# Kernel optimization log

Hardware: AMD Instinct MI355X
Metric: run time of the kernel (lower is better)

Reference implementation:

```python
import jax, jax.numpy as jnp
import numpy as np

B, T, D = 2, 2048, 2048
H, HD = 16, 128          # n_heads, head_dim = d_out // n_heads
DC, DR = 512, 64         # latent dim d_c, rope dim d_R


def _rope(x):
    """RoPE over last dim (even), positions along axis -2. x: [..., T, Dr]."""
    half = x.shape[-1] // 2
    t = x.shape[-2]
    inv_freq = 1.0 / (10000.0 ** (jnp.arange(half, dtype=jnp.float32) / half))
    freqs = jnp.arange(t, dtype=jnp.float32)[:, None] * inv_freq[None, :]  # [T, half]
    sin, cos = jnp.sin(freqs), jnp.cos(freqs)
    x1, x2 = x[..., :half], x[..., half:]
    # stack pairs on a new last axis then flatten -> interleaved layout,
    # matching torch.stack((...), dim=-1) followed by implicit flatten
    rot = jnp.stack([x1 * cos - x2 * sin, x1 * sin + x2 * cos], axis=-1)
    return rot.reshape(x.shape[:-1] + (2 * half,))


def setup_inputs() -> dict:
    key = jax.random.key(0)
    ks = jax.random.split(key, 10)
    s = 0.02  # init scale
    return {
        "x":     jax.random.normal(ks[0], (B, T, D), dtype=jnp.float32),
        "W_DKV": jax.random.normal(ks[1], (D, DC), dtype=jnp.float32) * s,
        "W_DQ":  jax.random.normal(ks[2], (D, DC), dtype=jnp.float32) * s,
        "W_UK":  jax.random.normal(ks[3], (DC, D), dtype=jnp.float32) * s,
        "W_UV":  jax.random.normal(ks[4], (DC, D), dtype=jnp.float32) * s,
        "W_UQ":  jax.random.normal(ks[5], (DC, D), dtype=jnp.float32) * s,
        "W_KR":  jax.random.normal(ks[6], (D, DR), dtype=jnp.float32) * s,
        "W_QR":  jax.random.normal(ks[7], (DC, H * DR), dtype=jnp.float32) * s,
        "W_O":   jax.random.normal(ks[8], (D, D), dtype=jnp.float32) * s,
        "b_O":   jax.random.normal(ks[9], (D,), dtype=jnp.float32) * s,
    }


def reference(x, W_DKV, W_DQ, W_UK, W_UV, W_UQ, W_KR, W_QR, W_O, b_O):
    b, t, d = x.shape
    # latent KV compression and up-projection
    c_kv = x @ W_DKV                                        # [B,T,d_c]
    K = (c_kv @ W_UK).reshape(b, t, H, HD).transpose(0, 2, 1, 3)  # [B,H,T,hd]
    V = (c_kv @ W_UV).reshape(b, t, H, HD).transpose(0, 2, 1, 3)
    # latent Q compression and up-projection
    c_q = x @ W_DQ                                          # [B,T,d_c]
    Q = (c_q @ W_UQ).reshape(b, t, H, HD).transpose(0, 2, 1, 3)
    # decoupled RoPE channels: shared rotary key per token, per-head rotary query
    k_R = _rope(x @ W_KR)[:, None, :, :]                    # [B,1,T,d_R]
    k_R = jnp.broadcast_to(k_R, (b, H, t, DR))
    q_R = (c_q @ W_QR).reshape(b, t, H, DR).transpose(0, 2, 1, 3)  # [B,H,T,d_R]
    q_R = _rope(q_R)
    # concat content + rotary channels
    Kf = jnp.concatenate([K, k_R], axis=-1)                 # [B,H,T,hd+d_R]
    Qf = jnp.concatenate([Q, q_R], axis=-1)
    scale = 1.0 / jnp.sqrt(jnp.float32(HD + DR))
    scores = jnp.einsum('bhqd,bhkd->bhqk', Qf, Kf) * scale  # [B,H,T,T]
    attn = jax.nn.softmax(scores, axis=-1)                  # dropout is identity (p=0 / eval)
    ctx = jnp.einsum('bhqk,bhkd->bhqd', attn, V)            # [B,H,T,hd]
    ctx = ctx.transpose(0, 2, 1, 3).reshape(b, t, d)
    return ctx @ W_O + b_O
```

## Files before the change

kernel.cpp:

```cpp
#include <hip/hip_runtime.h>
#include <hip/hip_bf16.h>

typedef __attribute__((ext_vector_type(8))) short short8;
typedef __attribute__((ext_vector_type(4))) short s4_t;
typedef __attribute__((ext_vector_type(4))) float f32x4;
typedef __attribute__((ext_vector_type(16))) float f32x16;
typedef __attribute__((ext_vector_type(2))) unsigned uint2v;
typedef __hip_bfloat16 bf16;

#define NB 2
#define NT 2048
#define NDIM 2048
#define NH 16
#define NHD 128
#define NDC 512
#define NDR 64

__device__ __forceinline__ void gl_lds16(const bf16* g, bf16* l){
  __builtin_amdgcn_global_load_lds(
      (const __attribute__((address_space(1))) void*)(const void*)g,
      (__attribute__((address_space(3))) void*)(void*)l, 16, 0, 0);
}

static __device__ inline unsigned cvtpk(float lo, float hi){
  unsigned u;
  asm("v_cvt_pk_bf16_f32 %0, %1, %2" : "=v"(u) : "v"(lo), "v"(hi));
  return u;
}

__global__ __launch_bounds__(256) void cvt_kernel(const float* __restrict__ src, bf16* __restrict__ dst){
  int i = (blockIdx.x*256 + threadIdx.x)*4;
  float4 v = *(const float4*)(src + i);
  dst[i+0] = __float2bfloat16(v.x);
  dst[i+1] = __float2bfloat16(v.y);
  dst[i+2] = __float2bfloat16(v.z);
  dst[i+3] = __float2bfloat16(v.w);
}

struct TAll {
  const float* src[8];
  bf16* dst[8];
  int K[8];
  int N[8];
  int cum[9];
};
__global__ __launch_bounds__(256) void tconv_all(TAll a){
  __shared__ float tile[32][33];
  int bid = blockIdx.x;
  int i = 0;
  #pragma unroll
  for (int j=0;j<8;j++) if (bid >= a.cum[j+1]) i = j+1;
  const float* W = a.src[i];
  bf16* Wt = a.dst[i];
  int K = a.K[i], N = a.N[i];
  int tl = bid - a.cum[i];
  int ntx = N >> 5;
  int n0 = (tl % ntx)*32, k0 = (tl / ntx)*32;
  int tx = threadIdx.x & 31, ty = threadIdx.x >> 5;
  #pragma unroll
  for (int j=0;j<32;j+=8) tile[ty+j][tx] = W[(size_t)(k0+ty+j)*N + n0 + tx];
  __syncthreads();
  #pragma unroll
  for (int j=0;j<32;j+=8) Wt[(size_t)(n0+ty+j)*K + k0 + tx] = __float2bfloat16(tile[tx][ty+j]);
}

template<int MODE>
__global__ __launch_bounds__(256,3) void gemm_bt(const bf16* __restrict__ A,
    const bf16* __restrict__ Bt, bf16* __restrict__ C, bf16* __restrict__ C2,
    float* __restrict__ Cf, const float* __restrict__ bias,
    int M, int N, int K, int lda, float mult)
{
  __shared__ bf16 As[128*64];
  __shared__ bf16 Bs[128*64];
  const int m0 = blockIdx.x*128, n0 = blockIdx.y*128;
  const int t = threadIdx.x, lane = t&63, w = t>>6;
  const int wr = w>>1, wc = w&1;
  const int l15 = lane&15, lg = lane>>4;
  const int wbase = t & 192;

  f32x4 acc[4][4];
  #pragma unroll
  for (int mi=0;mi<4;mi++)
    #pragma unroll
    for (int nj=0;nj<4;nj++) acc[mi][nj] = (f32x4){0.f,0.f,0.f,0.f};

  for (int k0=0;k0<K;k0+=64){
    __syncthreads();
    #pragma unroll
    for (int j=0;j<4;j++){
      int c = j*256 + t;
      int r = c>>3, cc = (c&7)*8;
      gl_lds16(A + (size_t)(m0+r)*lda + k0 + cc, As + (size_t)(j*256 + wbase)*8);
      int bn = n0 + r; if (bn > N-1) bn = N-1;
      gl_lds16(Bt + (size_t)bn*K + k0 + cc, Bs + (size_t)(j*256 + wbase)*8);
    }
    __syncthreads();
    #pragma unroll
    for (int kk=0;kk<2;kk++){
      short8 af[4], bfv[4];
      #pragma unroll
      for (int mi=0;mi<4;mi++) af[mi] = *(const short8*)&As[(wr*64+mi*16+l15)*64 + kk*32+lg*8];
      #pragma unroll
      for (int nj=0;nj<4;nj++) bfv[nj] = *(const short8*)&Bs[(wc*64+nj*16+l15)*64 + kk*32+lg*8];
      #pragma unroll
      for (int mi=0;mi<4;mi++)
        #pragma unroll
        for (int nj=0;nj<4;nj++)
          acc[mi][nj] = __builtin_amdgcn_mfma_f32_16x16x32_bf16(af[mi], bfv[nj], acc[mi][nj], 0,0,0);
    }
  }

  if constexpr (MODE==5){
    if (n0 >= 2048){
      int qh = (n0 - 2048 + wc*64) >> 6;
      int bidx = m0 >> 11;
      size_t hb = ((size_t)bidx*NH + qh)*(size_t)NT;
      float invf[2];
      invf[0] = __expf(-(float)l15 * 0.2878231366242557f);
      invf[1] = __expf(-(float)(16 + l15) * 0.2878231366242557f);
      #pragma unroll
      for (int mi=0;mi<4;mi++){
        #pragma unroll
        for (int r2=0;r2<4;r2++){
          int tp = (m0 & 2047) + wr*64 + mi*16 + lg*4 + r2;
          #pragma unroll
          for (int bb2=0;bb2<2;bb2++){
            float x1 = acc[mi][bb2][r2];
            float x2 = acc[mi][bb2+2][r2];
            float fr = (float)tp * invf[bb2];
            float sn, cs;
            sincosf(fr, &sn, &cs);
            float o0 = (x1*cs - x2*sn)*mult;
            float o1 = (x1*sn + x2*cs)*mult;
            int i2 = (bb2<<4) + l15;
            *(unsigned*)&C[(hb + tp)*192 + 128 + 2*i2] = cvtpk(o0, o1);
          }
        }
      }
      return;
    }
  }
  #pragma unroll
  for (int mi=0;mi<4;mi++){
    #pragma unroll
    for (int nj=0;nj<4;nj++){
      f32x4 v = acc[mi][nj];
      int gr0 = m0 + wr*64 + mi*16 + lg*4;
      int gc  = n0 + wc*64 + nj*16 + l15;
      if constexpr (MODE==0){
        if (gc < N){
          #pragma unroll
          for (int r2=0;r2<4;r2++) C[(size_t)(gr0+r2)*N + gc] = __float2bfloat16(v[r2]*mult);
        }
      } else if constexpr (MODE==2){
        float bb = bias[gc];
        #pragma unroll
        for (int r2=0;r2<4;r2++) Cf[(size_t)(gr0+r2)*N + gc] = v[r2]*mult + bb;
      } else if constexpr (MODE==4){
        int bidx = m0 >> 11;
        int tl0 = (m0 & 2047) + wr*64 + mi*16 + lg*4;
        if (gc < 2048){
          int hq = gc >> 7, dl = gc & 127;
          size_t base = ((size_t)bidx*NH + hq)*(size_t)NT;
          #pragma unroll
          for (int r2=0;r2<4;r2++) C[(base + tl0 + r2)*192 + dl] = __float2bfloat16(v[r2]);
        } else {
          int g2 = gc - 2048;
          int hq = g2 >> 7, dl = g2 & 127;
          s4_t pk;
          #pragma unroll
          for (int r2=0;r2<4;r2++){
            union { bf16 b; unsigned short u; } cvu;
            cvu.b = __float2bfloat16(v[r2]);
            pk[r2] = (short)cvu.u;
          }
          *(s4_t*)&C2[(((size_t)bidx*NH + hq)*NHD + dl)*NT + tl0] = pk;
        }
      } else {
        int bidx = m0 >> 11;
        int tl0 = (m0 & 2047) + wr*64 + mi*16 + lg*4;
        int hq = gc >> 7, dl = gc & 127;
        size_t base = ((size_t)bidx*NH + hq)*(size_t)NT;
        #pragma unroll
        for (int r2=0;r2<4;r2++) C[(base + tl0 + r2)*192 + dl] = __float2bfloat16(v[r2]*mult);
      }
    }
  }
}

__global__ __launch_bounds__(128) void rope_k(const bf16* __restrict__ krp,
    bf16* __restrict__ Kf)
{
  int bt = blockIdx.x*2 + (threadIdx.x>>6);
  int d = threadIdx.x & 63;
  int b = bt >> 11, tpos = bt & 2047;
  int i = d >> 1;
  float inv = __expf(-(float)i * 0.2878231366242557f);
  float fr = (float)tpos * inv;
  float sn, cs;
  sincosf(fr, &sn, &cs);

  float x1 = __bfloat162float(krp[(size_t)bt*1088 + i]);
  float x2 = __bfloat162float(krp[(size_t)bt*1088 + 32 + i]);
  float kv = (d&1) ? (x1*sn + x2*cs) : (x1*cs - x2*sn);
  bf16 kvb = __float2bfloat16(kv);
  size_t base = ((size_t)b*NH*NT + tpos)*192;
  #pragma unroll
  for (int h=0;h<NH;h++) Kf[base + (size_t)h*NT*192 + 128 + d] = kvb;
}

static __device__ inline void plswap(unsigned &a, unsigned &b){
  uint2v r = __builtin_amdgcn_permlane32_swap(a, b, false, false);
  a = r[0]; b = r[1];
}

__global__ __launch_bounds__(256,2) void attn_kernel(const bf16* __restrict__ Qf,
    const bf16* __restrict__ Kf, const bf16* __restrict__ Vt, bf16* __restrict__ ctx)
{
  __shared__ __align__(16) char smem[81920];

  const int lin = blockIdx.x;
  const int swz = (lin & 7)*64 + (lin >> 3);
  const int qt = swz & 15, bh = swz >> 4;
  const int b = bh >> 4, h = bh & 15;
  const int q0 = qt * 128;
  const int t = threadIdx.x, lane = t&63, w = t>>6;
  const int l31 = lane&31, hi = lane>>5;
  const int rsw = (l31&7)<<4;
  const int hib = hi*16;

  const bf16* Qp  = Qf + ((size_t)bh*NT + q0)*192;
  const bf16* Kp  = Kf + (size_t)bh*NT*192;
  const bf16* Vtp = Vt + (size_t)bh*NHD*NT;

  short8 qf[12];
  #pragma unroll
  for (int kk=0;kk<12;kk++)
    qf[kk] = *(const short8*)(Qp + (size_t)(w*32 + l31)*192 + kk*16 + hi*8);

  f32x16 o[4];
  #pragma unroll
  for (int Dt=0;Dt<4;Dt++)
    #pragma unroll
    for (int r=0;r<16;r++) o[Dt][r] = 0.f;
  float mrun = -1e30f, lrun = 0.f;

  short8 kst[6], vst[4];
  auto load_tile = [&](int kt){
    const bf16* Ksrc = Kp + (size_t)kt*64*192;
    #pragma unroll
    for (int j=0;j<6;j++) kst[j] = *(const short8*)(Ksrc + (j*256+t)*8);
    #pragma unroll
    for (int j=0;j<4;j++){
      int c = j*256 + t;
      vst[j] = *(const short8*)(Vtp + (size_t)(c>>3)*NT + kt*64 + (c&7)*8);
    }
  };
  load_tile(0);

  for (int kt=0; kt<NT/64; kt++){
    char* KsB  = smem + (kt&1)*40960;
    char* VTsB = KsB + 24576;
    #pragma unroll
    for (int j=0;j<6;j++){
      int c = j*256 + t;
      int r = c/24, cb = (c%24)*16;
      *(short8*)(KsB + r*384 + (cb ^ ((r&7)<<4))) = kst[j];
    }
    #pragma unroll
    for (int j=0;j<4;j++){
      int c = j*256 + t;
      int r = c>>3, cb = (c&7)*16;
      *(short8*)(VTsB + r*128 + (cb ^ ((r&7)<<4))) = vst[j];
    }
    if (kt+1 < NT/64) load_tile(kt+1);
    __syncthreads();

    f32x16 sa[2];
    #pragma unroll
    for (int Mt=0;Mt<2;Mt++)
      #pragma unroll
      for (int r=0;r<16;r++) sa[Mt][r] = 0.f;
    __builtin_amdgcn_s_setprio(1);
    #pragma unroll
    for (int kk=0;kk<12;kk++){
      int cb = kk*32 + hib;
      short8 kf0 = *(const short8*)(KsB + (size_t)l31*384        + ((cb) ^ rsw));
      short8 kf1 = *(const short8*)(KsB + (size_t)(l31+32)*384   + ((cb) ^ rsw));
      sa[0] = __builtin_amdgcn_mfma_f32_32x32x16_bf16(kf0, qf[kk], sa[0], 0,0,0);
      sa[1] = __builtin_amdgcn_mfma_f32_32x32x16_bf16(kf1, qf[kk], sa[1], 0,0,0);
    }
    __builtin_amdgcn_s_setprio(0);

    float mx[8];
    #pragma unroll
    for (int i2=0;i2<8;i2++)
      mx[i2] = fmaxf(fmaxf(sa[0][2*i2], sa[0][2*i2+1]), fmaxf(sa[1][2*i2], sa[1][2*i2+1]));
    float tm = fmaxf(fmaxf(fmaxf(mx[0],mx[1]),fmaxf(mx[2],mx[3])),
                     fmaxf(fmaxf(mx[4],mx[5]),fmaxf(mx[6],mx[7])));
    tm = fmaxf(tm, __shfl_xor(tm, 32));

    if (__any(tm > mrun + 8.f)){
      float mn = fmaxf(mrun, tm);
      float alpha = __expf(mrun - mn);
      mrun = mn;
      lrun *= alpha;
      #pragma unroll
      for (int Dt=0;Dt<4;Dt++)
        #pragma unroll
        for (int r=0;r<16;r++) o[Dt][r] *= alpha;
    }

    #pragma unroll
    for (int Mt=0;Mt<2;Mt++)
      #pragma unroll
      for (int r=0;r<16;r++) sa[Mt][r] = __expf(sa[Mt][r] - mrun);
    float sm[8];
    #pragma unroll
    for (int i2=0;i2<8;i2++)
      sm[i2] = (sa[0][2*i2] + sa[0][2*i2+1]) + (sa[1][2*i2] + sa[1][2*i2+1]);
    float rs = ((sm[0]+sm[1])+(sm[2]+sm[3])) + ((sm[4]+sm[5])+(sm[6]+sm[7]));
    rs += __shfl_xor(rs, 32);
    lrun += rs;

    short8 pf[4];
    #pragma unroll
    for (int Mt=0;Mt<2;Mt++){
      unsigned u[8];
      #pragma unroll
      for (int p8=0;p8<8;p8++) u[p8] = cvtpk(sa[Mt][2*p8], sa[Mt][2*p8+1]);
      plswap(u[0], u[2]); plswap(u[1], u[3]);
      plswap(u[4], u[6]); plswap(u[5], u[7]);
      union { unsigned du[4]; short8 s8; } f0, f1;
      f0.du[0]=u[0]; f0.du[1]=u[1]; f0.du[2]=u[2]; f0.du[3]=u[3];
      f1.du[0]=u[4]; f1.du[1]=u[5]; f1.du[2]=u[6]; f1.du[3]=u[7];
      pf[2*Mt+0] = f0.s8;
      pf[2*Mt+1] = f1.s8;
    }

    __builtin_amdgcn_s_setprio(1);
    #pragma unroll
    for (int kw=0;kw<4;kw++){
      int cb = kw*32 + hib;
      #pragma unroll
      for (int Dt=0;Dt<4;Dt++){
        short8 vf = *(const short8*)(VTsB + (size_t)(Dt*32 + l31)*128 + ((cb) ^ rsw));
        o[Dt] = __builtin_amdgcn_mfma_f32_32x32x16_bf16(vf, pf[kw], o[Dt], 0,0,0);
      }
    }
    __builtin_amdgcn_s_setprio(0);
  }

  __syncthreads();
  float il = 1.0f / lrun;
  bf16* Es = (bf16*)smem;
  const int EROW = 136;
  const int ebase = w*32*EROW;
  #pragma unroll
  for (int Dt=0;Dt<4;Dt++)
    #pragma unroll
    for (int r=0;r<16;r++){
      int d = Dt*32 + (r&3) + 8*(r>>2) + 4*hi;
      Es[ebase + l31*EROW + d] = __float2bfloat16(o[Dt][r]*il);
    }
  __syncthreads();
  int q = lane>>1, halfd = lane&1;
  size_t gq = q0 + w*32 + q;
  size_t obase = (((size_t)b*NT + gq)*NH + h)*NHD + halfd*64;
  #pragma unroll
  for (int pp=0;pp<8;pp++)
    *(short8*)&ctx[obase + pp*8] = *(short8*)&Es[ebase + q*EROW + halfd*64 + pp*8];
}

extern "C" void kernel_launch(void* const* d_in, const int* in_sizes, int n_in,
                              void* d_out, int out_size, void* d_ws, size_t ws_size,
                              hipStream_t stream)
{
  const float* x     = (const float*)d_in[0];
  const float* W_DKV = (const float*)d_in[1];
  const float* W_DQ  = (const float*)d_in[2];
  const float* W_UK  = (const float*)d_in[3];
  const float* W_UV  = (const float*)d_in[4];
  const float* W_UQ  = (const float*)d_in[5];
  const float* W_KR  = (const float*)d_in[6];
  const float* W_QR  = (const float*)d_in[7];
  const float* W_O   = (const float*)d_in[8];
  const float* b_O   = (const float*)d_in[9];

  const float scale = 0.07216878364870323f;

  char* ws = (char*)d_ws;
  bf16* xb    = (bf16*)(ws + 0);
  bf16* wcomb = (bf16*)(ws + 16777216);
  bf16* wuk   = (bf16*)(ws + 21233664);
  bf16* wuv   = (bf16*)(ws + 23330816);
  bf16* wuq   = (bf16*)(ws + 25427968);
  bf16* wqr   = (bf16*)(ws + 27525120);
  bf16* wo    = (bf16*)(ws + 28573696);
  bf16* comb  = (bf16*)(ws + 36962304);
  bf16* Qf    = (bf16*)(ws + 54263808);
  bf16* Kf    = (bf16*)(ws + 79429632);
  bf16* vt    = (bf16*)(ws + 104595456);
  bf16* ctxb  = (bf16*)(ws + 121372672);

  bf16* ckv = comb;
  bf16* cq  = comb + 512;
  bf16* krp = comb + 1024;

  cvt_kernel<<<8192,256,0,stream>>>(x, xb);

  TAll ta;
  ta.src[0]=W_DKV; ta.dst[0]=wcomb;             ta.K[0]=2048; ta.N[0]=512;
  ta.src[1]=W_DQ;  ta.dst[1]=wcomb + 512*2048;  ta.K[1]=2048; ta.N[1]=512;
  ta.src[2]=W_KR;  ta.dst[2]=wcomb + 1024*2048; ta.K[2]=2048; ta.N[2]=64;
  ta.src[3]=W_UK;  ta.dst[3]=wuk;               ta.K[3]=512;  ta.N[3]=2048;
  ta.src[4]=W_UV;  ta.dst[4]=wuv;               ta.K[4]=512;  ta.N[4]=2048;
  ta.src[5]=W_UQ;  ta.dst[5]=wuq;               ta.K[5]=512;  ta.N[5]=2048;
  ta.src[6]=W_QR;  ta.dst[6]=wqr;               ta.K[6]=512;  ta.N[6]=1024;
  ta.src[7]=W_O;   ta.dst[7]=wo;                ta.K[7]=2048; ta.N[7]=2048;
  ta.cum[0]=0;
  for (int i=0;i<8;i++) ta.cum[i+1] = ta.cum[i] + (ta.N[i]/32)*(ta.K[i]/32);
  tconv_all<<<ta.cum[8],256,0,stream>>>(ta);

  gemm_bt<0><<<dim3(32,9), 256,0,stream>>>(xb, wcomb, comb, nullptr, nullptr, nullptr, 4096, 1088, 2048, 2048, 1.0f);

  rope_k<<<2048,128,0,stream>>>(krp, Kf);

  gemm_bt<4><<<dim3(32,32),256,0,stream>>>(ckv, wuk, Kf, vt, nullptr, nullptr, 4096, 4096, 512, 1088, 1.0f);
  gemm_bt<5><<<dim3(32,24),256,0,stream>>>(cq, wuq, Qf, nullptr, nullptr, nullptr, 4096, 3072, 512, 1088, scale);

  attn_kernel<<<512,256,0,stream>>>(Qf, Kf, vt, ctxb);
  gemm_bt<2><<<dim3(32,16),256,0,stream>>>(ctxb, wo, nullptr, nullptr, (float*)d_out, b_O, 4096, 2048, 2048, 2048, 1.0f);
}
```

Before: 272.5 us.

## Store V in MFMA-fragment layout and load it directly from global

The projection epilogue now writes V^T in a pre-tiled layout that matches the MFMA B-operand fragment order per 64-key tile. The attention kernel loads V fragments straight from global/L2 into registers, with no LDS staging, and shrinks shared memory to hold only the double-buffered K tile. This removes the LDS writes and reads for V and frees shared memory. In exchange, each of the four waves now issues its own global loads for the same V data, so V traffic through L2 goes up. It also costs 16 more vector registers per thread, which could reduce occupancy, and the global load latency is less hidden.

```diff
diff --git a/kernel.cpp b/kernel.cpp
--- a/kernel.cpp
+++ b/kernel.cpp
@@ -167,6 +167,7 @@
         } else {
           int g2 = gc - 2048;
           int hq = g2 >> 7, dl = g2 & 127;
+          int kt = tl0 >> 6, kw = (tl0>>4)&3, hi2 = (tl0>>3)&1, j0 = tl0&7;
           s4_t pk;
           #pragma unroll
           for (int r2=0;r2<4;r2++){
@@ -174,7 +175,8 @@
             cvu.b = __float2bfloat16(v[r2]);
             pk[r2] = (short)cvu.u;
           }
-          *(s4_t*)&C2[(((size_t)bidx*NH + hq)*NHD + dl)*NT + tl0] = pk;
+          size_t base = (((size_t)(bidx*NH + hq)*32 + kt)*8 + kw*2 + hi2)*1024 + dl*8 + j0;
+          *(s4_t*)&C2[base] = pk;
         }
       } else {
         int bidx = m0 >> 11;
@@ -217,7 +219,7 @@
 __global__ __launch_bounds__(256,2) void attn_kernel(const bf16* __restrict__ Qf,
     const bf16* __restrict__ Kf, const bf16* __restrict__ Vt, bf16* __restrict__ ctx)
 {
-  __shared__ __align__(16) char smem[81920];
+  __shared__ __align__(16) char smem[49152];
 
   const int lin = blockIdx.x;
   const int swz = (lin & 7)*64 + (lin >> 3);
@@ -245,36 +247,32 @@
     for (int r=0;r<16;r++) o[Dt][r] = 0.f;
   float mrun = -1e30f, lrun = 0.f;
 
-  short8 kst[6], vst[4];
-  auto load_tile = [&](int kt){
+  short8 kst[6];
+  auto load_k = [&](int kt){
     const bf16* Ksrc = Kp + (size_t)kt*64*192;
     #pragma unroll
     for (int j=0;j<6;j++) kst[j] = *(const short8*)(Ksrc + (j*256+t)*8);
-    #pragma unroll
-    for (int j=0;j<4;j++){
-      int c = j*256 + t;
-      vst[j] = *(const short8*)(Vtp + (size_t)(c>>3)*NT + kt*64 + (c&7)*8);
-    }
   };
-  load_tile(0);
+  load_k(0);
 
   for (int kt=0; kt<NT/64; kt++){
-    char* KsB  = smem + (kt&1)*40960;
-    char* VTsB = KsB + 24576;
+    char* KsB = smem + (kt&1)*24576;
     #pragma unroll
     for (int j=0;j<6;j++){
       int c = j*256 + t;
       int r = c/24, cb = (c%24)*16;
       *(short8*)(KsB + r*384 + (cb ^ ((r&7)<<4))) = kst[j];
     }
-    #pragma unroll
-    for (int j=0;j<4;j++){
-      int c = j*256 + t;
-      int r = c>>3, cb = (c&7)*16;
-      *(short8*)(VTsB + r*128 + (cb ^ ((r&7)<<4))) = vst[j];
-    }
-    if (kt+1 < NT/64) load_tile(kt+1);
     __syncthreads();
+
+    if (kt+1 < NT/64) load_k(kt+1);
+    const bf16* Vb2 = Vtp + (size_t)kt*8192;
+    short8 vf[16];
+    #pragma unroll
+    for (int kw=0;kw<4;kw++)
+      #pragma unroll
+      for (int Dt=0;Dt<4;Dt++)
+        vf[kw*4+Dt] = *(const short8*)(Vb2 + (kw*2+hi)*1024 + (Dt*32+l31)*8);
 
     f32x16 sa[2];
     #pragma unroll
@@ -341,12 +339,9 @@
     __builtin_amdgcn_s_setprio(1);
     #pragma unroll
     for (int kw=0;kw<4;kw++){
-      int cb = kw*32 + hib;
-      #pragma unroll
-      for (int Dt=0;Dt<4;Dt++){
-        short8 vf = *(const short8*)(VTsB + (size_t)(Dt*32 + l31)*128 + ((cb) ^ rsw));
-        o[Dt] = __builtin_amdgcn_mfma_f32_32x32x16_bf16(vf, pf[kw], o[Dt], 0,0,0);
-      }
+      #pragma unroll
+      for (int Dt=0;Dt<4;Dt++)
+        o[Dt] = __builtin_amdgcn_mfma_f32_32x32x16_bf16(vf[kw*4+Dt], pf[kw], o[Dt], 0,0,0);
     }
     __builtin_amdgcn_s_setprio(0);
   }
```

Result: slower. 313.9 us (+15.2%).

## Stage K/V tiles with direct global-to-LDS loads instead of register staging

Applied to the files above, without the earlier changes.

The attention kernel now loads K and transposed-V tiles straight into shared memory with global_load_lds, instead of loading into registers and then writing to LDS. The XOR swizzle moves from the LDS write address to the permuted global source address, so the LDS layout seen by the MFMA reads stays the same. The next tile is issued into the other double buffer at the top of each iteration, and the barrier moves to the end of the loop. This removes about 40 staging VGPRs and the explicit LDS store instructions. It relies on the barrier waiting for the outstanding async loads, and the source-side swizzle makes global access less contiguous.

```diff
diff --git a/kernel.cpp b/kernel.cpp
--- a/kernel.cpp
+++ b/kernel.cpp
@@ -217,7 +217,7 @@
 __global__ __launch_bounds__(256,2) void attn_kernel(const bf16* __restrict__ Qf,
     const bf16* __restrict__ Kf, const bf16* __restrict__ Vt, bf16* __restrict__ ctx)
 {
-  __shared__ __align__(16) char smem[81920];
+  __shared__ __align__(16) bf16 smem[40960];
 
   const int lin = blockIdx.x;
   const int swz = (lin & 7)*64 + (lin >> 3);
@@ -228,6 +228,7 @@
   const int l31 = lane&31, hi = lane>>5;
   const int rsw = (l31&7)<<4;
   const int hib = hi*16;
+  const int wbase = t & 192;
 
   const bf16* Qp  = Qf + ((size_t)bh*NT + q0)*192;
   const bf16* Kp  = Kf + (size_t)bh*NT*192;
@@ -245,36 +246,30 @@
     for (int r=0;r<16;r++) o[Dt][r] = 0.f;
   float mrun = -1e30f, lrun = 0.f;
 
-  short8 kst[6], vst[4];
-  auto load_tile = [&](int kt){
+  auto stage = [&](int kt, bf16* buf){
     const bf16* Ksrc = Kp + (size_t)kt*64*192;
     #pragma unroll
-    for (int j=0;j<6;j++) kst[j] = *(const short8*)(Ksrc + (j*256+t)*8);
+    for (int j=0;j<6;j++){
+      int c = j*256 + t;
+      int r = c/24, ce = (c%24)*8;
+      gl_lds16(Ksrc + (size_t)r*192 + (ce ^ ((r&7)<<3)), buf + (size_t)(j*256 + wbase)*8);
+    }
+    bf16* vb = buf + 12288;
     #pragma unroll
     for (int j=0;j<4;j++){
       int c = j*256 + t;
-      vst[j] = *(const short8*)(Vtp + (size_t)(c>>3)*NT + kt*64 + (c&7)*8);
+      int r = c>>3, ce = (c&7)*8;
+      gl_lds16(Vtp + (size_t)r*NT + kt*64 + (ce ^ ((r&7)<<3)), vb + (size_t)(j*256 + wbase)*8);
     }
   };
-  load_tile(0);
+
+  stage(0, smem);
+  __syncthreads();
 
   for (int kt=0; kt<NT/64; kt++){
-    char* KsB  = smem + (kt&1)*40960;
-    char* VTsB = KsB + 24576;
-    #pragma unroll
-    for (int j=0;j<6;j++){
-      int c = j*256 + t;
-      int r = c/24, cb = (c%24)*16;
-      *(short8*)(KsB + r*384 + (cb ^ ((r&7)<<4))) = kst[j];
-    }
-    #pragma unroll
-    for (int j=0;j<4;j++){
-      int c = j*256 + t;
-      int r = c>>3, cb = (c&7)*16;
-      *(short8*)(VTsB + r*128 + (cb ^ ((r&7)<<4))) = vst[j];
-    }
-    if (kt+1 < NT/64) load_tile(kt+1);
-    __syncthreads();
+    const char* KsB  = (const char*)(smem + (kt&1)*20480);
+    const char* VTsB = KsB + 24576;
+    if (kt+1 < NT/64) stage(kt+1, smem + ((kt+1)&1)*20480);
 
     f32x16 sa[2];
     #pragma unroll
@@ -349,11 +344,11 @@
       }
     }
     __builtin_amdgcn_s_setprio(0);
+    __syncthreads();
   }
 
-  __syncthreads();
   float il = 1.0f / lrun;
-  bf16* Es = (bf16*)smem;
+  bf16* Es = smem;
   const int EROW = 136;
   const int ebase = w*32*EROW;
   #pragma unroll
```

Result: no change. 270.1 us (-0.9%).
